# Performance work log

Measured on AMD Instinct MI355X. Metric: run time of the kernel, lower is better.

The kernel has to match this reference:

```python
import jax, jax.numpy as jnp
import numpy as np

# dims
B, S, D = 2, 4096, 1024
H, d, R, K, CH = 16, 64, 48, 4, 256


def causal_dwconv(x, w):
    # x: [B,S,C], w: [C,K] depthwise causal conv (torch Conv1d pad=K-1, keep first S)
    Kk = w.shape[1]
    xp = jnp.pad(x, ((0, 0), (Kk - 1, 0), (0, 0)))
    out = jnp.zeros_like(x)
    for j in range(Kk):
        out = out + w[:, j] * xp[:, j:j + x.shape[1], :]
    return out


def rmsnorm(x, w, eps=1e-6):
    return x * jax.lax.rsqrt(jnp.mean(x * x, axis=-1, keepdims=True) + eps) * w


def setup_inputs():
    key = jax.random.key(0)
    ks = jax.random.split(key, 16)
    rn = lambda k, shape, std=0.02: jax.random.normal(k, shape, jnp.float32) * std
    return {
        'x': jax.random.normal(ks[0], (B, S, D), jnp.float32),
        'Wq': rn(ks[1], (D, D)), 'Wk': rn(ks[2], (D, D)), 'Wv': rn(ks[3], (D, D)),
        'Wo': rn(ks[4], (D, D)),
        'conv_q': rn(ks[5], (D, K), 0.25), 'conv_k': rn(ks[6], (D, K), 0.25),
        'conv_v': rn(ks[7], (D, K), 0.25),
        'Wf': rn(ks[8], (D, H)), 'bf': jnp.full((H,), 2.0, jnp.float32),
        'Wl': rn(ks[9], (D, H)), 'bl': jnp.zeros((H,), jnp.float32),
        'Wrq': rn(ks[10], (D, H * R), 0.01), 'Wrk': rn(ks[11], (D, H * R), 0.01),
        'graph_scale': rn(ks[12], (H,), 0.1),
        'qn_w': jnp.ones((d,), jnp.float32), 'kn_w': jnp.ones((d,), jnp.float32),
        'on_w': jnp.ones((D,), jnp.float32),
    }


def _forward(x, Wq, Wk, Wv, Wo, conv_q, conv_k, conv_v, Wf, bf, Wl, bl, Wrq, Wrk,
             graph_scale, qn_w, kn_w, on_w):
    Bb, Ss, Dd = x.shape
    # proj + depthwise causal short conv, split heads -> [B,H,S,d]
    q = causal_dwconv(x @ Wq, conv_q).reshape(Bb, Ss, H, d).transpose(0, 2, 1, 3)
    k = causal_dwconv(x @ Wk, conv_k).reshape(Bb, Ss, H, d).transpose(0, 2, 1, 3)
    v = causal_dwconv(x @ Wv, conv_v).reshape(Bb, Ss, H, d).transpose(0, 2, 1, 3)
    q = rmsnorm(q, qn_w)
    k = rmsnorm(k, kn_w)
    # low-rank relative terms, zero-padded from R to d
    Rq = (x @ Wrq).reshape(Bb, Ss, H, R).transpose(0, 2, 1, 3)
    Rk = (x @ Wrk).reshape(Bb, Ss, H, R).transpose(0, 2, 1, 3)
    Rq = jnp.pad(Rq, ((0, 0), (0, 0), (0, 0), (0, d - R)))
    Rk = jnp.pad(Rk, ((0, 0), (0, 0), (0, 0), (0, d - R)))
    lam = jnp.abs(graph_scale)[None, :, None, None]
    ksum = k + lam * Rk
    k_tilde = ksum / jnp.clip(jnp.linalg.norm(ksum, axis=-1, keepdims=True), 1e-12)
    q_tilde = q + lam * Rq
    alpha = jax.nn.sigmoid(x @ Wf + bf).transpose(0, 2, 1)  # [B,H,S]
    beta = jax.nn.sigmoid(x @ Wl + bl).transpose(0, 2, 1)
    # gated delta-rule scan: mem[B,H,d,d]
    mem0 = jnp.zeros((Bb, H, d, d), x.dtype)
    nC = Ss // CH
    to_t = lambda a: a.transpose(2, 0, 1, 3).reshape(nC, CH, Bb, H, d)
    to_s = lambda a: a.transpose(2, 0, 1).reshape(nC, CH, Bb, H)
    xs = (to_t(k_tilde), to_t(v), to_t(q_tilde), to_s(alpha), to_s(beta))

    def step(mem, inp):
        k_t, v_t, q_t, a_t, b_t = inp
        retrieved = jnp.einsum('bhij,bhj->bhi', mem, k_t)
        delta = v_t - retrieved
        mem = a_t[..., None, None] * mem + b_t[..., None, None] * (delta[..., None] * k_t[..., None, :])
        out_t = jnp.einsum('bhij,bhj->bhi', mem, q_t)
        return mem, out_t

    def chunk_step(mem, inp):
        mem2, outs = jax.lax.scan(step, mem, inp)
        # original python scan detaches memory at chunk boundaries
        return jax.lax.stop_gradient(mem2), outs

    _, outs = jax.lax.scan(chunk_step, mem0, xs)  # [nC,CH,B,H,d]
    out = outs.reshape(Ss, Bb, H, d).transpose(1, 0, 2, 3).reshape(Bb, Ss, Dd)
    out = rmsnorm(out, on_w)
    return out @ Wo


def reference(x, Wq, Wk, Wv, Wo, conv_q, conv_k, conv_v, Wf, bf, Wl, bl, Wrq, Wrk,
              graph_scale, qn_w, kn_w, on_w):
    return _forward(x, Wq, Wk, Wv, Wo, conv_q, conv_k, conv_v, Wf, bf, Wl, bl,
                    Wrq, Wrk, graph_scale, qn_w, kn_w, on_w)
```

## Files before the change

kernel.cpp:

```cpp
#include <hip/hip_runtime.h>


typedef __attribute__((ext_vector_type(8))) short short8;
typedef __attribute__((ext_vector_type(4))) float f32x4;

#define B_ 2
#define S_ 4096
#define D_ 1024
#define H_ 16
#define R_ 48
#define M_ 8192
#define CW 16
#define NCH (S_ / CW)

__device__ __forceinline__ unsigned short f2bf(float f) {
  unsigned u = __float_as_uint(f);
  u += 0x7FFFu + ((u >> 16) & 1u);
  return (unsigned short)(u >> 16);
}
__device__ __forceinline__ float bf2f(unsigned short u) {
  return __uint_as_float(((unsigned)u) << 16);
}

__device__ __forceinline__ void lbar() {
  __builtin_amdgcn_sched_barrier(0);
  asm volatile("s_waitcnt lgkmcnt(0)" ::: "memory");
  __builtin_amdgcn_s_barrier();
  __builtin_amdgcn_sched_barrier(0);
}

#define GLDS16(g, l) __builtin_amdgcn_global_load_lds(                        \
    (const __attribute__((address_space(1))) unsigned int*)(g),              \
    (__attribute__((address_space(3))) unsigned int*)(l), 16, 0, 0)

__global__ __launch_bounds__(256) void cast_bf16_kernel(
    const float* __restrict__ in, unsigned short* __restrict__ out, int n4) {
  int i = blockIdx.x * 256 + threadIdx.x;
  for (; i < n4; i += gridDim.x * 256) {
    float4 v = ((const float4*)in)[i];
    ushort4 o;
    o.x = f2bf(v.x); o.y = f2bf(v.y); o.z = f2bf(v.z); o.w = f2bf(v.w);
    ((ushort4*)out)[i] = o;
  }
}

__global__ void transpose_w_kernel(const float* __restrict__ W,
                                   unsigned short* __restrict__ Wt,
                                   int Kd, int N) {
  __shared__ float tile[32][33];
  int n0 = blockIdx.x * 32, k0 = blockIdx.y * 32;
  int tx = threadIdx.x, ty = threadIdx.y;
#pragma unroll
  for (int i = 0; i < 32; i += 8)
    tile[ty + i][tx] = W[(size_t)(k0 + ty + i) * N + n0 + tx];
  __syncthreads();
#pragma unroll
  for (int i = 0; i < 32; i += 8)
    Wt[(size_t)(n0 + ty + i) * Kd + k0 + tx] = f2bf(tile[tx][ty + i]);
}

__global__ __launch_bounds__(256) void pack_wfl_kernel(
    const float* __restrict__ Wf, const float* __restrict__ Wl,
    unsigned short* __restrict__ wfl) {
  int o = blockIdx.x * 256 + threadIdx.x;
  int j = o >> 10, k = o & 1023;
  float v = (j < 16) ? Wf[k * 16 + j] : Wl[k * 16 + (j - 16)];
  wfl[o] = f2bf(v);
}

template <bool BF16OUT>
__global__ __launch_bounds__(256) void gemm_bt_kernel(
    const unsigned short* __restrict__ A, const unsigned short* __restrict__ Bt,
    void* __restrict__ Cv, int M, int N, int Kd) {
  __shared__ alignas(16) unsigned short lds[2 * 128 * 64];
  unsigned short* ldsA = lds;
  unsigned short* ldsB = lds + 128 * 64;
  int tid = threadIdx.x;
  int wave = tid >> 6, lane = tid & 63;
  int nBlocks = N >> 7;
  int bm = blockIdx.x / nBlocks, bn = blockIdx.x % nBlocks;
  int m0 = bm << 7, n0 = bn << 7;
  int wm = (wave >> 1) << 6, wn = (wave & 1) << 6;

  f32x4 acc[4][4] = {};

  int rowInChunk = lane >> 3;
  int kOff = (lane & 7) * 8;

  const unsigned short* Abase = A + (size_t)m0 * Kd;
  const unsigned short* Bbase = Bt + (size_t)n0 * Kd;

  for (int k0 = 0; k0 < Kd; k0 += 64) {
    __syncthreads();
#pragma unroll
    for (int r = 0; r < 4; r++) {
      int c = wave * 4 + r;
      int row = c * 8 + rowInChunk;
      GLDS16(Abase + (size_t)row * Kd + k0 + kOff, ldsA + c * 512);
    }
#pragma unroll
    for (int r = 0; r < 4; r++) {
      int c = wave * 4 + r;
      int row = c * 8 + rowInChunk;
      GLDS16(Bbase + (size_t)row * Kd + k0 + kOff, ldsB + c * 512);
    }
    asm volatile("s_waitcnt vmcnt(0)" ::: "memory");
    __syncthreads();
#pragma unroll
    for (int kk = 0; kk < 2; kk++) {
      short8 af[4], bfr[4];
      int kb = kk * 32 + (lane >> 4) * 8;
#pragma unroll
      for (int i = 0; i < 4; i++) {
        int ar = wm + i * 16 + (lane & 15);
        af[i] = *(const short8*)(ldsA + ar * 64 + kb);
        int br = wn + i * 16 + (lane & 15);
        bfr[i] = *(const short8*)(ldsB + br * 64 + kb);
      }
#pragma unroll
      for (int i = 0; i < 4; i++)
#pragma unroll
        for (int j = 0; j < 4; j++)
          acc[i][j] = __builtin_amdgcn_mfma_f32_16x16x32_bf16(
              af[i], bfr[j], acc[i][j], 0, 0, 0);
    }
  }
  int cr = (lane >> 4) * 4;
  int cc = lane & 15;
#pragma unroll
  for (int i = 0; i < 4; i++)
#pragma unroll
    for (int j = 0; j < 4; j++)
#pragma unroll
      for (int rg = 0; rg < 4; rg++) {
        int row = m0 + wm + i * 16 + cr + rg;
        int col = n0 + wn + j * 16 + cc;
        if (BF16OUT)
          ((unsigned short*)Cv)[(size_t)row * N + col] = f2bf(acc[i][j][rg]);
        else
          ((float*)Cv)[(size_t)row * N + col] = acc[i][j][rg];
      }
}

__global__ __launch_bounds__(256) void fl_gemm_kernel(
    const unsigned short* __restrict__ xb, const unsigned short* __restrict__ wfl,
    const float* __restrict__ bfv, const float* __restrict__ blv,
    float* __restrict__ alpha, float* __restrict__ beta) {
  __shared__ alignas(16) unsigned short ldsA[128 * 64];
  __shared__ alignas(16) unsigned short ldsB[32 * 64];
  int tid = threadIdx.x, wave = tid >> 6, lane = tid & 63;
  int m0 = blockIdx.x << 7;
  f32x4 acc[2][2] = {};
  int rowInChunk = lane >> 3, kOff = (lane & 7) * 8;
  const unsigned short* Abase = xb + (size_t)m0 * 1024;

  for (int k0 = 0; k0 < 1024; k0 += 64) {
    __syncthreads();
#pragma unroll
    for (int r = 0; r < 4; r++) {
      int ch = wave * 4 + r;
      int row = ch * 8 + rowInChunk;
      GLDS16(Abase + (size_t)row * 1024 + k0 + kOff, ldsA + ch * 512);
    }
    {
      int row = wave * 8 + rowInChunk;
      GLDS16(wfl + (size_t)row * 1024 + k0 + kOff, ldsB + wave * 512);
    }
    asm volatile("s_waitcnt vmcnt(0)" ::: "memory");
    __syncthreads();
#pragma unroll
    for (int kk = 0; kk < 2; kk++) {
      int kb2 = kk * 32 + (lane >> 4) * 8;
      short8 af[2], bfr[2];
#pragma unroll
      for (int i = 0; i < 2; i++)
        af[i] = *(const short8*)(ldsA + (wave * 32 + i * 16 + (lane & 15)) * 64 + kb2);
#pragma unroll
      for (int j = 0; j < 2; j++)
        bfr[j] = *(const short8*)(ldsB + (j * 16 + (lane & 15)) * 64 + kb2);
#pragma unroll
      for (int i = 0; i < 2; i++)
#pragma unroll
        for (int j = 0; j < 2; j++)
          acc[i][j] = __builtin_amdgcn_mfma_f32_16x16x32_bf16(
              af[i], bfr[j], acc[i][j], 0, 0, 0);
    }
  }
  int cr = (lane >> 4) * 4, cc = lane & 15;
#pragma unroll
  for (int i = 0; i < 2; i++)
#pragma unroll
    for (int j = 0; j < 2; j++)
#pragma unroll
      for (int rg = 0; rg < 4; rg++) {
        int row = m0 + wave * 32 + i * 16 + cr + rg;
        int col = j * 16 + cc;
        float z = acc[i][j][rg] + ((col < 16) ? bfv[col] : blv[col - 16]);
        float s = 1.f / (1.f + __expf(-z));
        int bb = row >> 12, tt = row & 4095, hh = col & 15;
        float* dst = (col < 16) ? alpha : beta;
        dst[((size_t)(bb * 16 + hh)) * 4096 + tt] = s;
      }
}

__global__ __launch_bounds__(256) void prep_kernel(
    const unsigned short* __restrict__ xqkv, const unsigned short* __restrict__ rqk,
    const float* __restrict__ cq, const float* __restrict__ ck,
    const float* __restrict__ cv, const float* __restrict__ gs,
    const float* __restrict__ qnw, const float* __restrict__ knw,
    unsigned short* __restrict__ qt, unsigned short* __restrict__ kt,
    unsigned short* __restrict__ vc) {
  int m = blockIdx.x;
  int b = m >> 12, t = m & 4095;
  int tid = threadIdx.x;
  int c4 = tid << 2;
  int h = c4 >> 6;
  int j4 = c4 & 63;

  float wq[4][4], wk[4][4], wv[4][4];
#pragma unroll
  for (int u = 0; u < 4; u++) {
    *(float4*)wq[u] = *(const float4*)(cq + (c4 + u) * 4);
    *(float4*)wk[u] = *(const float4*)(ck + (c4 + u) * 4);
    *(float4*)wv[u] = *(const float4*)(cv + (c4 + u) * 4);
  }
  float qv[4] = {0, 0, 0, 0}, kv[4] = {0, 0, 0, 0}, vv[4] = {0, 0, 0, 0};
#pragma unroll
  for (int j = 0; j < 4; j++) {
    int tt = t + j - 3;
    if (tt < 0) continue;
    const unsigned short* xr = xqkv + ((size_t)((b << 12) + tt)) * 3072;
    ushort4 uq = *(const ushort4*)(xr + c4);
    ushort4 uk = *(const ushort4*)(xr + 1024 + c4);
    ushort4 uv = *(const ushort4*)(xr + 2048 + c4);
    float xq[4] = {bf2f(uq.x), bf2f(uq.y), bf2f(uq.z), bf2f(uq.w)};
    float xk[4] = {bf2f(uk.x), bf2f(uk.y), bf2f(uk.z), bf2f(uk.w)};
    float xv[4] = {bf2f(uv.x), bf2f(uv.y), bf2f(uv.z), bf2f(uv.w)};
#pragma unroll
    for (int u = 0; u < 4; u++) {
      qv[u] = fmaf(wq[u][j], xq[u], qv[u]);
      kv[u] = fmaf(wk[u][j], xk[u], kv[u]);
      vv[u] = fmaf(wv[u][j], xv[u], vv[u]);
    }
  }
  float ssq = qv[0] * qv[0] + qv[1] * qv[1] + qv[2] * qv[2] + qv[3] * qv[3];
  ssq += __shfl_xor(ssq, 1); ssq += __shfl_xor(ssq, 2);
  ssq += __shfl_xor(ssq, 4); ssq += __shfl_xor(ssq, 8);
  float qsc = rsqrtf(ssq * (1.f / 64.f) + 1e-6f);
  float ssk = kv[0] * kv[0] + kv[1] * kv[1] + kv[2] * kv[2] + kv[3] * kv[3];
  ssk += __shfl_xor(ssk, 1); ssk += __shfl_xor(ssk, 2);
  ssk += __shfl_xor(ssk, 4); ssk += __shfl_xor(ssk, 8);
  float ksc = rsqrtf(ssk * (1.f / 64.f) + 1e-6f);

  float lam = fabsf(gs[h]);
  float rq[4] = {0, 0, 0, 0}, rk[4] = {0, 0, 0, 0};
  if (j4 < R_) {
    const unsigned short* rr = rqk + (size_t)m * 1536;
    ushort4 uq = *(const ushort4*)(rr + h * R_ + j4);
    ushort4 uk = *(const ushort4*)(rr + 768 + h * R_ + j4);
    rq[0] = bf2f(uq.x); rq[1] = bf2f(uq.y); rq[2] = bf2f(uq.z); rq[3] = bf2f(uq.w);
    rk[0] = bf2f(uk.x); rk[1] = bf2f(uk.y); rk[2] = bf2f(uk.z); rk[3] = bf2f(uk.w);
  }
  float qtv[4], ksum[4];
#pragma unroll
  for (int u = 0; u < 4; u++) {
    float qn = qv[u] * qsc * qnw[j4 + u];
    float kn = kv[u] * ksc * knw[j4 + u];
    qtv[u] = fmaf(lam, rq[u], qn);
    ksum[u] = fmaf(lam, rk[u], kn);
  }
  float ss2 = ksum[0] * ksum[0] + ksum[1] * ksum[1] + ksum[2] * ksum[2] +
              ksum[3] * ksum[3];
  ss2 += __shfl_xor(ss2, 1); ss2 += __shfl_xor(ss2, 2);
  ss2 += __shfl_xor(ss2, 4); ss2 += __shfl_xor(ss2, 8);
  float inv = 1.f / fmaxf(sqrtf(ss2), 1e-12f);

  size_t ob = ((size_t)((b * 16 + h) * 4096 + t)) * 64 + j4;
  ushort4 oq, ok, ov;
  oq.x = f2bf(qtv[0]); oq.y = f2bf(qtv[1]); oq.z = f2bf(qtv[2]); oq.w = f2bf(qtv[3]);
  ok.x = f2bf(ksum[0] * inv); ok.y = f2bf(ksum[1] * inv);
  ok.z = f2bf(ksum[2] * inv); ok.w = f2bf(ksum[3] * inv);
  ov.x = f2bf(vv[0]); ov.y = f2bf(vv[1]); ov.z = f2bf(vv[2]); ov.w = f2bf(vv[3]);
  *(ushort4*)(qt + ob) = oq;
  *(ushort4*)(kt + ob) = ok;
  *(ushort4*)(vc + ob) = ov;
}

__global__ __launch_bounds__(64) void wy_pre_kernel(
    const unsigned short* __restrict__ qt, const unsigned short* __restrict__ kt,
    const float* __restrict__ al, const float* __restrict__ be,
    unsigned short* __restrict__ Tw, unsigned short* __restrict__ Mw,
    float* __restrict__ Gw, unsigned short* __restrict__ KTw) {
  __shared__ float g5[5][16];
  __shared__ float Af[16][17];
  __shared__ unsigned short Tb[16][16];
  int tile = blockIdx.x;
  int bh = tile >> 8, c = tile & 255;
  int tg = c * CW;
  int l = threadIdx.x;

  const unsigned short* kb = kt + (size_t)bh * S_ * 64 + (size_t)tg * 64;
  const unsigned short* qb = qt + (size_t)bh * S_ * 64 + (size_t)tg * 64;

  float a_ = 1.f, bt_ = 0.f;
  if (l < 16) {
    a_ = al[(size_t)bh * S_ + tg + l];
    bt_ = be[(size_t)bh * S_ + tg + l];
  }
  float la = __log2f(a_);
  float pre = la;
  {
    float y;
    y = __shfl_up(pre, 1);  if (l >= 1) pre += y;
    y = __shfl_up(pre, 2);  if (l >= 2) pre += y;
    y = __shfl_up(pre, 4);  if (l >= 4) pre += y;
    y = __shfl_up(pre, 8);  if (l >= 8) pre += y;
  }
  float tot = __shfl(pre, 15);
  if (l < 16) {
    g5[0][l] = bt_;
    g5[1][l] = bt_ * exp2f(pre - la);
    g5[2][l] = exp2f(pre);
    g5[3][l] = exp2f(tot - pre);
    g5[4][l] = exp2f(-pre);
  }

  short8 kf0 = *(const short8*)(kb + (size_t)(l & 15) * 64 + (l >> 4) * 8);
  short8 kf1 = *(const short8*)(kb + (size_t)(l & 15) * 64 + 32 + (l >> 4) * 8);
  short8 qf0 = *(const short8*)(qb + (size_t)(l & 15) * 64 + (l >> 4) * 8);
  short8 qf1 = *(const short8*)(qb + (size_t)(l & 15) * 64 + 32 + (l >> 4) * 8);
  f32x4 aK = {0.f, 0.f, 0.f, 0.f}, aQ = {0.f, 0.f, 0.f, 0.f};
  aK = __builtin_amdgcn_mfma_f32_16x16x32_bf16(kf0, kf0, aK, 0, 0, 0);
  aK = __builtin_amdgcn_mfma_f32_16x16x32_bf16(kf1, kf1, aK, 0, 0, 0);
  aQ = __builtin_amdgcn_mfma_f32_16x16x32_bf16(qf0, kf0, aQ, 0, 0, 0);
  aQ = __builtin_amdgcn_mfma_f32_16x16x32_bf16(qf1, kf1, aQ, 0, 0, 0);

  {
    unsigned short* Ko = KTw + (size_t)tile * 1024 + (l & 15);
    int hi = l >> 4;
#pragma unroll
    for (int u = 0; u < 8; u++) {
      Ko[(hi * 8 + u) * 16] = (unsigned short)kf0[u];
      Ko[(32 + hi * 8 + u) * 16] = (unsigned short)kf1[u];
    }
  }

  __syncthreads();

  int s = l & 15;
  unsigned short* Mo = Mw + (size_t)tile * 256;
#pragma unroll
  for (int r = 0; r < 4; r++) {
    int t = (l >> 4) * 4 + r;
    Af[t][s] = (s < t) ? g5[1][t] * g5[4][s] * aK[r] : 0.f;
    float mv = (s <= t) ? g5[2][t] * g5[4][s] * aQ[r] : 0.f;
    Mo[t * 16 + s] = f2bf(mv);
  }
  __syncthreads();

  if (l < 16) {
    int j = l;
    float u[16];
#pragma unroll
    for (int t = 0; t < 16; t++) {
      float x = (t == j) ? 1.f : 0.f;
#pragma unroll
      for (int s2 = 0; s2 < 16; s2++) {
        if (s2 >= t) break;
        x = fmaf(-Af[t][s2], u[s2], x);
      }
      u[t] = x;
      Tb[t][j] = f2bf(x);
    }
  }
  __syncthreads();

  {
    ushort4 v = *(const ushort4*)&Tb[l >> 2][(l & 3) * 4];
    *(ushort4*)&Tw[(size_t)tile * 256 + l * 4] = v;
  }
  if (l < 64) Gw[(size_t)tile * 64 + l] = g5[l >> 4][l & 15];
}

__global__ __launch_bounds__(256, 1) void scan_wy_kernel(
    const unsigned short* __restrict__ qt, const unsigned short* __restrict__ kt,
    const unsigned short* __restrict__ vc, const unsigned short* __restrict__ Tw,
    const unsigned short* __restrict__ Mw, const float* __restrict__ Gw,
    const unsigned short* __restrict__ KTw, float* __restrict__ attn) {
  __shared__ alignas(16) unsigned short Kc[2][16][72];
  __shared__ alignas(16) unsigned short Qc[2][16][72];
  __shared__ alignas(16) unsigned short KT[2][64][40];
  __shared__ alignas(16) unsigned short Vc[2][16][24];
  __shared__ alignas(16) unsigned short Tl[2][16][40];
  __shared__ alignas(16) unsigned short Mb[2][16][40];
  __shared__ alignas(16) float G[2][64];
  __shared__ alignas(16) float SWq[16][20];
  __shared__ alignas(16) unsigned short Cb[16][40];
  __shared__ alignas(16) unsigned short Ubt[16][40];
  __shared__ alignas(16) unsigned short Udt[16][40];
  __shared__ alignas(16) unsigned short Sb[16][72];

  int blk = blockIdx.x;
  int bh = blk & 31, rg = blk >> 5;
  int b = bh >> 4, h = bh & 15;
  int tid = threadIdx.x;
  int w = tid >> 6, l = tid & 63;

  const unsigned short* kb = kt + (size_t)bh * S_ * 64;
  const unsigned short* qb = qt + (size_t)bh * S_ * 64;
  const unsigned short* vb = vc + (size_t)bh * S_ * 64 + rg * 16;
  const unsigned short* Tbg = Tw + (size_t)bh * 256 * 256;
  const unsigned short* Mbg = Mw + (size_t)bh * 256 * 256;
  const float* Gb = Gw + (size_t)bh * 256 * 64;
  const unsigned short* Kbg = KTw + (size_t)bh * 256 * 1024;
  float* ob = attn + (size_t)(b * S_) * 1024 + h * 64 + rg * 16;

  for (int i = tid; i < 16 * 72; i += 256) ((unsigned short*)Sb)[i] = 0;

  f32x4 Sreg = {0.f, 0.f, 0.f, 0.f};

  int trow = tid >> 4, ti = tid & 15;
  int jrow = tid >> 2, jq = tid & 3;
  ushort4 pk = *(const ushort4*)(kb + (size_t)trow * 64 + ti * 4);
  ushort4 pq = *(const ushort4*)(qb + (size_t)trow * 64 + ti * 4);
  unsigned short pv = vb[(size_t)trow * 64 + ti];
  unsigned short pt = Tbg[tid];
  unsigned short pm = Mbg[tid];
  ushort4 pkt = *(const ushort4*)(Kbg + tid * 4);
  float pg = (tid < 64) ? Gb[tid] : 0.f;

  lbar();

  for (int c = 0; c < NCH; ++c) {
    int p = c & 1;
    int tg0 = c * CW;
    *(ushort4*)&Kc[p][trow][ti * 4] = pk;
    *(ushort4*)&Qc[p][trow][ti * 4] = pq;
    *(ushort4*)&KT[p][jrow][jq * 4] = pkt;
    *(ushort4*)&KT[p][jrow][16 + jq * 4] = pkt;
    Vc[p][trow][ti] = pv;
    Tl[p][trow][ti] = pt;
    Tl[p][trow][16 + ti] = pt;
    Mb[p][trow][ti] = pm;
    Mb[p][trow][16 + ti] = pm;
    if (tid < 64) G[p][tid] = pg;
    if (c + 1 < NCH) {
      size_t cb = (size_t)(tg0 + CW) * 64;
      pk = *(const ushort4*)(kb + cb + (size_t)trow * 64 + ti * 4);
      pq = *(const ushort4*)(qb + cb + (size_t)trow * 64 + ti * 4);
      pv = vb[cb + (size_t)trow * 64 + ti];
      size_t t2 = (size_t)(c + 1) * 256;
      pt = Tbg[t2 + tid];
      pm = Mbg[t2 + tid];
      pkt = *(const ushort4*)(Kbg + (size_t)(c + 1) * 1024 + tid * 4);
      if (tid < 64) pg = Gb[(size_t)(c + 1) * 64 + tid];
    }
    lbar();

    if (w == 0) {
      short8 s0 = *(const short8*)&Sb[l & 15][(l >> 4) * 8];
      short8 s1 = *(const short8*)&Sb[l & 15][32 + (l >> 4) * 8];
      short8 b0 = *(const short8*)&Kc[p][l & 15][(l >> 4) * 8];
      short8 b1 = *(const short8*)&Kc[p][l & 15][32 + (l >> 4) * 8];
      f32x4 acc = {0.f, 0.f, 0.f, 0.f};
      acc = __builtin_amdgcn_mfma_f32_16x16x32_bf16(s0, b0, acc, 0, 0, 0);
      acc = __builtin_amdgcn_mfma_f32_16x16x32_bf16(s1, b1, acc, 0, 0, 0);
      int t = l & 15;
      float gb_ = G[p][t], bg_ = G[p][16 + t];
      ushort4 v4 = *(const ushort4*)&Vc[p][t][(l >> 4) * 4];
      unsigned short va[4] = {v4.x, v4.y, v4.z, v4.w};
#pragma unroll
      for (int r = 0; r < 4; r++) {
        int i = (l >> 4) * 4 + r;
        float c0 = gb_ * bf2f(va[r]) - bg_ * acc[r];
        unsigned short hi = f2bf(c0);
        Cb[i][t] = hi;
        Cb[i][16 + t] = f2bf(c0 - bf2f(hi));
      }
      short8 ta = *(const short8*)&Tl[p][l & 15][(l >> 4) * 8];
      short8 cbf = *(const short8*)&Cb[l & 15][(l >> 4) * 8];
      f32x4 ua = {0.f, 0.f, 0.f, 0.f};
      ua = __builtin_amdgcn_mfma_f32_16x16x32_bf16(ta, cbf, ua, 0, 0, 0);
      f32x4 gp4 = *(const f32x4*)&G[p][48 + (l >> 4) * 4];
      ushort4 uh, ulo, dh, dlo;
      unsigned short* uhp = &uh.x;
      unsigned short* ulp = &ulo.x;
      unsigned short* dhp = &dh.x;
      unsigned short* dlp = &dlo.x;
#pragma unroll
      for (int r = 0; r < 4; r++) {
        float uv = ua[r];
        unsigned short h1 = f2bf(uv);
        uhp[r] = h1;
        ulp[r] = f2bf(uv - bf2f(h1));
        float dv = uv * gp4[r];
        unsigned short h2 = f2bf(dv);
        dhp[r] = h2;
        dlp[r] = f2bf(dv - bf2f(h2));
      }
      *(ushort4*)&Ubt[l & 15][(l >> 4) * 4] = uh;
      *(ushort4*)&Ubt[l & 15][16 + (l >> 4) * 4] = ulo;
      *(ushort4*)&Udt[l & 15][(l >> 4) * 4] = dh;
      *(ushort4*)&Udt[l & 15][16 + (l >> 4) * 4] = dlo;
    } else if (w == 1) {
      short8 s0 = *(const short8*)&Sb[l & 15][(l >> 4) * 8];
      short8 s1 = *(const short8*)&Sb[l & 15][32 + (l >> 4) * 8];
      short8 b0 = *(const short8*)&Qc[p][l & 15][(l >> 4) * 8];
      short8 b1 = *(const short8*)&Qc[p][l & 15][32 + (l >> 4) * 8];
      f32x4 acc = {0.f, 0.f, 0.f, 0.f};
      acc = __builtin_amdgcn_mfma_f32_16x16x32_bf16(s0, b0, acc, 0, 0, 0);
      acc = __builtin_amdgcn_mfma_f32_16x16x32_bf16(s1, b1, acc, 0, 0, 0);
#pragma unroll
      for (int r = 0; r < 4; r++)
        SWq[(l >> 4) * 4 + r][l & 15] = acc[r];
    }
    lbar();

    if (w == 1) {
      short8 ma = *(const short8*)&Mb[p][l & 15][(l >> 4) * 8];
      short8 ub = *(const short8*)&Ubt[l & 15][(l >> 4) * 8];
      f32x4 oa = {0.f, 0.f, 0.f, 0.f};
      oa = __builtin_amdgcn_mfma_f32_16x16x32_bf16(ma, ub, oa, 0, 0, 0);
      f32x4 sq4 = *(const f32x4*)&SWq[l & 15][(l >> 4) * 4];
      f32x4 gm4 = *(const f32x4*)&G[p][32 + (l >> 4) * 4];
#pragma unroll
      for (int r = 0; r < 4; r++) {
        int t = (l >> 4) * 4 + r;
        ob[(size_t)(tg0 + t) * 1024 + (l & 15)] = oa[r] + gm4[r] * sq4[r];
      }
    }
    {
      float gE = G[p][32 + 15];
      short8 ud = *(const short8*)&Udt[l & 15][(l >> 4) * 8];
      short8 ktf = *(const short8*)&KT[p][16 * w + (l & 15)][(l >> 4) * 8];
      f32x4 ci;
#pragma unroll
      for (int r = 0; r < 4; r++) ci[r] = gE * Sreg[r];
      ci = __builtin_amdgcn_mfma_f32_16x16x32_bf16(ud, ktf, ci, 0, 0, 0);
      Sreg = ci;
#pragma unroll
      for (int r = 0; r < 4; r++)
        Sb[(l >> 4) * 4 + r][16 * w + (l & 15)] = f2bf(ci[r]);
    }
  }
}

__global__ __launch_bounds__(256) void rmsnorm_out_kernel(
    const float* __restrict__ attn, const float* __restrict__ onw,
    unsigned short* __restrict__ normed) {
  int m = blockIdx.x, tid = threadIdx.x;
  const float* row = attn + (size_t)m * 1024;
  float xv[4];
  *(float4*)xv = *(const float4*)(row + tid * 4);
  float ss = xv[0] * xv[0] + xv[1] * xv[1] + xv[2] * xv[2] + xv[3] * xv[3];
#pragma unroll
  for (int o = 1; o < 64; o <<= 1) ss += __shfl_xor(ss, o);
  __shared__ float wss[4];
  if ((tid & 63) == 0) wss[tid >> 6] = ss;
  __syncthreads();
  float tot = wss[0] + wss[1] + wss[2] + wss[3];
  float sc = rsqrtf(tot * (1.f / 1024.f) + 1e-6f);
  float wv[4];
  *(float4*)wv = *(const float4*)(onw + tid * 4);
  ushort4 o4;
  o4.x = f2bf(xv[0] * sc * wv[0]);
  o4.y = f2bf(xv[1] * sc * wv[1]);
  o4.z = f2bf(xv[2] * sc * wv[2]);
  o4.w = f2bf(xv[3] * sc * wv[3]);
  *(ushort4*)(normed + (size_t)m * 1024 + tid * 4) = o4;
}

extern "C" void kernel_launch(void* const* d_in, const int* in_sizes, int n_in,
                              void* d_out, int out_size, void* d_ws,
                              size_t ws_size, hipStream_t stream) {
  const float* x = (const float*)d_in[0];
  const float* Wq = (const float*)d_in[1];
  const float* Wk = (const float*)d_in[2];
  const float* Wv = (const float*)d_in[3];
  const float* Wo = (const float*)d_in[4];
  const float* conv_q = (const float*)d_in[5];
  const float* conv_k = (const float*)d_in[6];
  const float* conv_v = (const float*)d_in[7];
  const float* Wf = (const float*)d_in[8];
  const float* bfv = (const float*)d_in[9];
  const float* Wl = (const float*)d_in[10];
  const float* blv = (const float*)d_in[11];
  const float* gs = (const float*)d_in[14];
  const float* qn_w = (const float*)d_in[15];
  const float* kn_w = (const float*)d_in[16];
  const float* on_w = (const float*)d_in[17];

  char* ws = (char*)d_ws;
  size_t used = 0;
  auto alloc = [&](size_t bytes) -> void* {
    void* p = (void*)(ws + used);
    used += (bytes + 255) & ~(size_t)255;
    return p;
  };
  unsigned short* xb = (unsigned short*)alloc((size_t)M_ * D_ * 2);
  unsigned short* wqkv_t = (unsigned short*)alloc((size_t)3072 * 1024 * 2);
  unsigned short* wr_t = (unsigned short*)alloc((size_t)1536 * 1024 * 2);
  unsigned short* wo_t = (unsigned short*)alloc((size_t)1024 * 1024 * 2);
  unsigned short* wfl = (unsigned short*)alloc((size_t)32 * 1024 * 2);
  unsigned short* xqkv = (unsigned short*)alloc((size_t)M_ * 3072 * 2);
  unsigned short* rqk = (unsigned short*)alloc((size_t)M_ * 1536 * 2);
  unsigned short* qt = (unsigned short*)alloc((size_t)M_ * 1024 * 2);
  unsigned short* kt = (unsigned short*)alloc((size_t)M_ * 1024 * 2);
  unsigned short* vc = (unsigned short*)alloc((size_t)M_ * 1024 * 2);
  float* alpha = (float*)alloc((size_t)B_ * H_ * S_ * 4);
  float* beta = (float*)alloc((size_t)B_ * H_ * S_ * 4);
  float* attn = (float*)xqkv;
  unsigned short* normed = rqk;
  unsigned short* KTw = rqk;
  char* xbc = (char*)xb;
  unsigned short* Tw = (unsigned short*)xbc;
  unsigned short* Mw = (unsigned short*)(xbc + 4u * 1024 * 1024);
  float* Gw = (float*)(xbc + 8u * 1024 * 1024);

  if (used > ws_size) return;

  cast_bf16_kernel<<<2048, 256, 0, stream>>>(x, xb, M_ * D_ / 4);

  dim3 tb(32, 8);
  transpose_w_kernel<<<dim3(32, 32), tb, 0, stream>>>(Wq, wqkv_t, 1024, 1024);
  transpose_w_kernel<<<dim3(32, 32), tb, 0, stream>>>(
      Wk, wqkv_t + (size_t)1024 * 1024, 1024, 1024);
  transpose_w_kernel<<<dim3(32, 32), tb, 0, stream>>>(
      Wv, wqkv_t + (size_t)2048 * 1024, 1024, 1024);
  transpose_w_kernel<<<dim3(24, 32), tb, 0, stream>>>(
      (const float*)d_in[12], wr_t, 1024, 768);
  transpose_w_kernel<<<dim3(24, 32), tb, 0, stream>>>(
      (const float*)d_in[13], wr_t + (size_t)768 * 1024, 1024, 768);
  transpose_w_kernel<<<dim3(32, 32), tb, 0, stream>>>(Wo, wo_t, 1024, 1024);
  pack_wfl_kernel<<<128, 256, 0, stream>>>(Wf, Wl, wfl);

  gemm_bt_kernel<true><<<64 * 24, 256, 0, stream>>>(xb, wqkv_t, xqkv, M_, 3072, 1024);
  gemm_bt_kernel<true><<<64 * 12, 256, 0, stream>>>(xb, wr_t, rqk, M_, 1536, 1024);

  fl_gemm_kernel<<<64, 256, 0, stream>>>(xb, wfl, bfv, blv, alpha, beta);

  prep_kernel<<<M_, 256, 0, stream>>>(xqkv, rqk, conv_q, conv_k, conv_v, gs,
                                      qn_w, kn_w, qt, kt, vc);

  wy_pre_kernel<<<32 * 256, 64, 0, stream>>>(qt, kt, alpha, beta, Tw, Mw, Gw,
                                             KTw);

  scan_wy_kernel<<<128, 256, 0, stream>>>(qt, kt, vc, Tw, Mw, Gw, KTw, attn);

  rmsnorm_out_kernel<<<M_, 256, 0, stream>>>(attn, on_w, normed);

  gemm_bt_kernel<false><<<64 * 8, 256, 0, stream>>>(normed, wo_t, (float*)d_out,
                                                    M_, 1024, 1024);
}
```

Before: 522.7 us.

## Remove mid-chunk barrier by redundant per-wave U/D compute and double-buffered state

Each wave now recomputes the C and U/D chain itself in private shared buffers instead of wave 0 producing them for everyone. The state buffer Sb is double-buffered so the state update can write the next copy while the output path still reads the current one. Together these remove one block barrier per chunk from the serial scan. The output's Q·S term is now computed by wave 0 after the state update rather than by wave 1 beforehand. The cost is redundant MFMA and conversion work in every wave, plus relying on wave-local ordering of shared-memory writes and reads.

```diff
diff --git a/kernel.cpp b/kernel.cpp
--- a/kernel.cpp
+++ b/kernel.cpp
@@ -394,11 +394,10 @@
   __shared__ alignas(16) unsigned short Tl[2][16][40];
   __shared__ alignas(16) unsigned short Mb[2][16][40];
   __shared__ alignas(16) float G[2][64];
-  __shared__ alignas(16) float SWq[16][20];
-  __shared__ alignas(16) unsigned short Cb[16][40];
+  __shared__ alignas(16) unsigned short Cb[4][16][40];
   __shared__ alignas(16) unsigned short Ubt[16][40];
-  __shared__ alignas(16) unsigned short Udt[16][40];
-  __shared__ alignas(16) unsigned short Sb[16][72];
+  __shared__ alignas(16) unsigned short Udt[4][16][40];
+  __shared__ alignas(16) unsigned short Sb[2][16][72];
 
   int blk = blockIdx.x;
   int bh = blk & 31, rg = blk >> 5;
@@ -415,7 +414,7 @@
   const unsigned short* Kbg = KTw + (size_t)bh * 256 * 1024;
   float* ob = attn + (size_t)(b * S_) * 1024 + h * 64 + rg * 16;
 
-  for (int i = tid; i < 16 * 72; i += 256) ((unsigned short*)Sb)[i] = 0;
+  for (int i = tid; i < 2 * 16 * 72; i += 256) ((unsigned short*)Sb)[i] = 0;
 
   f32x4 Sreg = {0.f, 0.f, 0.f, 0.f};
 
@@ -433,6 +432,8 @@
 
   for (int c = 0; c < NCH; ++c) {
     int p = c & 1;
+    int sp = c & 1;
+    int sn = (c + 1) & 1;
     int tg0 = c * CW;
     *(ushort4*)&Kc[p][trow][ti * 4] = pk;
     *(ushort4*)&Qc[p][trow][ti * 4] = pq;
@@ -457,9 +458,9 @@
     }
     lbar();
 
-    if (w == 0) {
-      short8 s0 = *(const short8*)&Sb[l & 15][(l >> 4) * 8];
-      short8 s1 = *(const short8*)&Sb[l & 15][32 + (l >> 4) * 8];
+    {
+      short8 s0 = *(const short8*)&Sb[sp][l & 15][(l >> 4) * 8];
+      short8 s1 = *(const short8*)&Sb[sp][l & 15][32 + (l >> 4) * 8];
       short8 b0 = *(const short8*)&Kc[p][l & 15][(l >> 4) * 8];
       short8 b1 = *(const short8*)&Kc[p][l & 15][32 + (l >> 4) * 8];
       f32x4 acc = {0.f, 0.f, 0.f, 0.f};
@@ -474,11 +475,11 @@
         int i = (l >> 4) * 4 + r;
         float c0 = gb_ * bf2f(va[r]) - bg_ * acc[r];
         unsigned short hi = f2bf(c0);
-        Cb[i][t] = hi;
-        Cb[i][16 + t] = f2bf(c0 - bf2f(hi));
+        Cb[w][i][t] = hi;
+        Cb[w][i][16 + t] = f2bf(c0 - bf2f(hi));
       }
       short8 ta = *(const short8*)&Tl[p][l & 15][(l >> 4) * 8];
-      short8 cbf = *(const short8*)&Cb[l & 15][(l >> 4) * 8];
+      short8 cbf = *(const short8*)&Cb[w][l & 15][(l >> 4) * 8];
       f32x4 ua = {0.f, 0.f, 0.f, 0.f};
       ua = __builtin_amdgcn_mfma_f32_16x16x32_bf16(ta, cbf, ua, 0, 0, 0);
       f32x4 gp4 = *(const f32x4*)&G[p][48 + (l >> 4) * 4];
@@ -498,49 +499,44 @@
         dhp[r] = h2;
         dlp[r] = f2bf(dv - bf2f(h2));
       }
-      *(ushort4*)&Ubt[l & 15][(l >> 4) * 4] = uh;
-      *(ushort4*)&Ubt[l & 15][16 + (l >> 4) * 4] = ulo;
-      *(ushort4*)&Udt[l & 15][(l >> 4) * 4] = dh;
-      *(ushort4*)&Udt[l & 15][16 + (l >> 4) * 4] = dlo;
-    } else if (w == 1) {
-      short8 s0 = *(const short8*)&Sb[l & 15][(l >> 4) * 8];
-      short8 s1 = *(const short8*)&Sb[l & 15][32 + (l >> 4) * 8];
-      short8 b0 = *(const short8*)&Qc[p][l & 15][(l >> 4) * 8];
-      short8 b1 = *(const short8*)&Qc[p][l & 15][32 + (l >> 4) * 8];
-      f32x4 acc = {0.f, 0.f, 0.f, 0.f};
-      acc = __builtin_amdgcn_mfma_f32_16x16x32_bf16(s0, b0, acc, 0, 0, 0);
-      acc = __builtin_amdgcn_mfma_f32_16x16x32_bf16(s1, b1, acc, 0, 0, 0);
+      *(ushort4*)&Udt[w][l & 15][(l >> 4) * 4] = dh;
+      *(ushort4*)&Udt[w][l & 15][16 + (l >> 4) * 4] = dlo;
+      if (w == 0) {
+        *(ushort4*)&Ubt[l & 15][(l >> 4) * 4] = uh;
+        *(ushort4*)&Ubt[l & 15][16 + (l >> 4) * 4] = ulo;
+      }
+    }
+    {
+      float gE = G[p][32 + 15];
+      short8 ud = *(const short8*)&Udt[w][l & 15][(l >> 4) * 8];
+      short8 ktf = *(const short8*)&KT[p][16 * w + (l & 15)][(l >> 4) * 8];
+      f32x4 ci;
+#pragma unroll
+      for (int r = 0; r < 4; r++) ci[r] = gE * Sreg[r];
+      ci = __builtin_amdgcn_mfma_f32_16x16x32_bf16(ud, ktf, ci, 0, 0, 0);
+      Sreg = ci;
 #pragma unroll
       for (int r = 0; r < 4; r++)
-        SWq[(l >> 4) * 4 + r][l & 15] = acc[r];
-    }
-    lbar();
-
-    if (w == 1) {
+        Sb[sn][(l >> 4) * 4 + r][16 * w + (l & 15)] = f2bf(ci[r]);
+    }
+    if (w == 0) {
+      short8 qa0 = *(const short8*)&Qc[p][l & 15][(l >> 4) * 8];
+      short8 qa1 = *(const short8*)&Qc[p][l & 15][32 + (l >> 4) * 8];
+      short8 sb0 = *(const short8*)&Sb[sp][l & 15][(l >> 4) * 8];
+      short8 sb1 = *(const short8*)&Sb[sp][l & 15][32 + (l >> 4) * 8];
+      f32x4 sq = {0.f, 0.f, 0.f, 0.f};
+      sq = __builtin_amdgcn_mfma_f32_16x16x32_bf16(qa0, sb0, sq, 0, 0, 0);
+      sq = __builtin_amdgcn_mfma_f32_16x16x32_bf16(qa1, sb1, sq, 0, 0, 0);
       short8 ma = *(const short8*)&Mb[p][l & 15][(l >> 4) * 8];
       short8 ub = *(const short8*)&Ubt[l & 15][(l >> 4) * 8];
       f32x4 oa = {0.f, 0.f, 0.f, 0.f};
       oa = __builtin_amdgcn_mfma_f32_16x16x32_bf16(ma, ub, oa, 0, 0, 0);
-      f32x4 sq4 = *(const f32x4*)&SWq[l & 15][(l >> 4) * 4];
       f32x4 gm4 = *(const f32x4*)&G[p][32 + (l >> 4) * 4];
 #pragma unroll
       for (int r = 0; r < 4; r++) {
         int t = (l >> 4) * 4 + r;
-        ob[(size_t)(tg0 + t) * 1024 + (l & 15)] = oa[r] + gm4[r] * sq4[r];
-      }
-    }
-    {
-      float gE = G[p][32 + 15];
-      short8 ud = *(const short8*)&Udt[l & 15][(l >> 4) * 8];
-      short8 ktf = *(const short8*)&KT[p][16 * w + (l & 15)][(l >> 4) * 8];
-      f32x4 ci;
-#pragma unroll
-      for (int r = 0; r < 4; r++) ci[r] = gE * Sreg[r];
-      ci = __builtin_amdgcn_mfma_f32_16x16x32_bf16(ud, ktf, ci, 0, 0, 0);
-      Sreg = ci;
-#pragma unroll
-      for (int r = 0; r < 4; r++)
-        Sb[(l >> 4) * 4 + r][16 * w + (l & 15)] = f2bf(ci[r]);
+        ob[(size_t)(tg0 + t) * 1024 + (l & 15)] = oa[r] + gm4[r] * sq[r];
+      }
     }
   }
 }
```

Result: slower. 584.3 us (median of 2 runs) (+11.8%).
